# Kernel optimization log

Hardware: AMD Instinct MI355X
Metric: run time of the kernel (lower is better)

Reference implementation:

```python
import jax, jax.numpy as jnp
import numpy as np

N, D, K = 65536, 64, 128   # points, feature dim, n_clusters
BETA = 0.0                 # distance weighting exponent offset
EPS = 1e-8


def pairwise_distance(a, b):
    # euclidean distance matrix [n, k]
    d2 = jnp.sum(a * a, 1)[:, None] + jnp.sum(b * b, 1)[None, :] - 2.0 * (a @ b.T)
    return jnp.sqrt(jnp.maximum(d2, 0.0))


def approx_cluster_filling(dist, beta):
    # differentiable soft cluster filling: inverse-distance weights with exponent (1+beta),
    # normalized per point, averaged over points -> [K]
    w = (dist + EPS) ** (-(1.0 + beta))
    w = w / jnp.sum(w, axis=1, keepdims=True)
    return jnp.mean(w, axis=0)


def wasserstein_distance(a, b):
    # sort-based per-feature 1D Wasserstein-1 distance, averaged over features
    return jnp.mean(jnp.abs(jnp.sort(a, axis=0) - jnp.sort(b, axis=0)))


def setup_inputs():
    key = jax.random.key(0)
    k1, k2, k3 = jax.random.split(key, 3)
    x = jax.random.normal(k1, (N, D), jnp.float32)
    target = jax.random.normal(k2, (N, D), jnp.float32)
    cluster_centers = jax.random.normal(k3, (K, D), jnp.float32)
    # precomputed target-side cluster statistics (LossKMeans.__init__, detached)
    dist_t = pairwise_distance(target, cluster_centers)
    prediction_target = jnp.argmin(dist_t, axis=1).astype(jnp.int32)
    filling_target = approx_cluster_filling(dist_t, BETA)
    return {"x": x, "target": target, "cluster_centers": cluster_centers,
            "prediction_target": prediction_target, "filling_target": filling_target}


def reference(x, target, cluster_centers, prediction_target, filling_target):
    # cluster-filling MSE (differentiable soft assignment)
    dist_x = pairwise_distance(x, cluster_centers)
    loss_fil = jnp.mean((approx_cluster_filling(dist_x, BETA) - filling_target) ** 2)
    # hard (detached) cluster assignment of x; concrete in eager mode
    pred_x = np.asarray(jnp.argmin(dist_x, axis=1))
    pred_t = np.asarray(prediction_target)
    loss_med = jnp.zeros((), jnp.float32)
    for c in np.unique(pred_x):  # data-dependent loop over occupied clusters (<= K)
        ix = np.nonzero(pred_x == c)[0]
        it = np.nonzero(pred_t == c)[0]
        m = min(ix.size, it.size)
        if m == 0:
            continue  # no matching target members -> skip (empty slices)
        loss_med = loss_med + wasserstein_distance(x[ix[:m]], target[it[:m]])
    return loss_fil + loss_med
```

## Files before the change

### kernel.cpp

```cpp
#include <hip/hip_runtime.h>
#include <math.h>

#define N_PTS 65536
#define DIM   64
#define K_CL  128
#define EPSV  1e-8f
#define CAP   8192


__global__ __launch_bounds__(256) void k_init(
    float* __restrict__ fill_acc, float* __restrict__ sumw,
    unsigned long long* __restrict__ pred_enc) {
  const int i = blockIdx.x * 256 + threadIdx.x;
  if (i < K_CL) fill_acc[i] = 0.0f;
  sumw[i] = 0.0f;
  pred_enc[i] = 0xFFFFFFFFFFFFFFFFull;
}

__global__ __launch_bounds__(256) void k_dist1(
    const float* __restrict__ x, const float* __restrict__ centers,
    float* __restrict__ sumw, unsigned long long* __restrict__ pred_enc,
    float* __restrict__ w)
{
  __shared__ float csq[32];
  const int kb    = blockIdx.x & 3;
  const int pb    = blockIdx.x >> 2;
  const int jbase = kb << 5;
  const int tid   = threadIdx.x;
  const int p     = pb * 256 + tid;

  if (tid < 32) {
    const float* cp = centers + (jbase + tid) * DIM;
    float s = 0.0f;
    #pragma unroll 8
    for (int d = 0; d < DIM; ++d) { float v = cp[d]; s += v * v; }
    csq[tid] = s;
  }

  float xr[DIM];
  const float4* xp = reinterpret_cast<const float4*>(x + (size_t)p * DIM);
  #pragma unroll
  for (int q = 0; q < DIM / 4; ++q) {
    float4 v = xp[q];
    xr[4 * q + 0] = v.x; xr[4 * q + 1] = v.y;
    xr[4 * q + 2] = v.z; xr[4 * q + 3] = v.w;
  }
  float xsq = 0.0f;
  #pragma unroll
  for (int d = 0; d < DIM; ++d) xsq += xr[d] * xr[d];
  __syncthreads();

  float sw = 0.0f, best = INFINITY;
  int   bj = jbase;
  #pragma unroll 2
  for (int jj = 0; jj < 32; ++jj) {
    const int j = jbase + jj;
    const float* cp = centers + j * DIM;
    float d0 = 0.f, d1 = 0.f, d2a = 0.f, d3 = 0.f;
    #pragma unroll
    for (int d = 0; d < DIM; d += 4) {
      d0  += xr[d + 0] * cp[d + 0];
      d1  += xr[d + 1] * cp[d + 1];
      d2a += xr[d + 2] * cp[d + 2];
      d3  += xr[d + 3] * cp[d + 3];
    }
    float dot  = (d0 + d1) + (d2a + d3);
    float dsq  = xsq + csq[jj] - 2.0f * dot;
    float dist = sqrtf(fmaxf(dsq, 0.0f));
    float ww   = 1.0f / (dist + EPSV);
    w[(size_t)j * N_PTS + p] = ww;
    sw += ww;
    if (dist < best) { best = dist; bj = j; }
  }
  atomicAdd(&sumw[p], sw);
  const unsigned long long enc =
      ((unsigned long long)__float_as_uint(best) << 32) | (unsigned int)bj;
  atomicMin(&pred_enc[p], enc);
}

__global__ __launch_bounds__(256) void k_pred(
    const unsigned long long* __restrict__ pred_enc,
    const float* __restrict__ sumw,
    int* __restrict__ pred_x, float* __restrict__ inv_sumw) {
  const int p = blockIdx.x * 256 + threadIdx.x;
  pred_x[p]   = (int)(pred_enc[p] & 0xFFFFFFFFull);
  inv_sumw[p] = 1.0f / sumw[p];
}

__global__ __launch_bounds__(256) void k_fill(
    const float* __restrict__ w, const float* __restrict__ inv_sumw,
    float* __restrict__ fill_acc)
{
  __shared__ float red[4];
  const int j    = blockIdx.x >> 3;
  const int seg  = blockIdx.x & 7;
  const int tid  = threadIdx.x;
  const float4* wj = reinterpret_cast<const float4*>(
      w + (size_t)j * N_PTS + seg * 8192);
  const float4* iv = reinterpret_cast<const float4*>(inv_sumw + seg * 8192);
  float s = 0.0f;
  #pragma unroll
  for (int q = 0; q < 8; ++q) {
    const int e = q * 256 + tid;
    float4 a = wj[e];
    float4 b = iv[e];
    s += a.x * b.x + a.y * b.y + a.z * b.z + a.w * b.w;
  }
  #pragma unroll
  for (int off = 32; off > 0; off >>= 1) s += __shfl_down(s, off);
  if ((tid & 63) == 0) red[tid >> 6] = s;
  __syncthreads();
  if (tid == 0)
    atomicAdd(&fill_acc[j], red[0] + red[1] + red[2] + red[3]);
}

__global__ __launch_bounds__(1024) void k_scatter(
    const int* __restrict__ pred_x, const int* __restrict__ pred_t,
    int* __restrict__ idx_x, int* __restrict__ idx_t,
    int* __restrict__ count_x, int* __restrict__ count_t)
{
  const int c    = blockIdx.x >> 1;
  const int side = blockIdx.x & 1;
  const int* __restrict__ pred = side ? pred_t : pred_x;
  int* __restrict__ out = side ? idx_t : idx_x;
  int* __restrict__ cnt = side ? count_t : count_x;

  __shared__ int wsum[16];
  const int tid = threadIdx.x, lane = tid & 63, w = tid >> 6;
  const int beg = w * 4096;

  int cw = 0;
  for (int s = 0; s < 4096; s += 64) {
    const bool m = (pred[beg + s + lane] == c);
    cw += __popcll(__ballot(m));
  }
  if (lane == 0) wsum[w] = cw;
  __syncthreads();
  int base = 0, tot = 0;
  #pragma unroll
  for (int k = 0; k < 16; ++k) { int v = wsum[k]; tot += v; if (k < w) base += v; }

  int run = base;
  for (int s = 0; s < 4096; s += 64) {
    const int i = beg + s + lane;
    const bool m = (pred[i] == c);
    unsigned long long bal = __ballot(m);
    int lp = __popcll(bal & ((1ull << lane) - 1ull));
    if (m) { int pos = run + lp; if (pos < CAP) out[c * CAP + pos] = i; }
    run += __popcll(bal);
  }
  if (tid == 0) cnt[c] = tot;
}

__global__ __launch_bounds__(128) void k_offsets(
    const int* __restrict__ count_x, const int* __restrict__ count_t,
    int* __restrict__ offc)
{
  __shared__ int sm[128];
  const int tid = threadIdx.x;
  const int m  = min(min(count_x[tid], CAP), min(count_t[tid], CAP));
  const int sz = ((m + 3) & ~3) * DIM;
  sm[tid] = sz;
  __syncthreads();
  for (int s = 1; s < 128; s <<= 1) {
    int v = (tid >= s) ? sm[tid - s] : 0;
    __syncthreads();
    sm[tid] += v;
    __syncthreads();
  }
  offc[tid] = sm[tid] - sz;
}

__global__ __launch_bounds__(256) void k_gather_t(
    const float* __restrict__ x, const float* __restrict__ t,
    const int* __restrict__ idx_x, const int* __restrict__ idx_t,
    const int* __restrict__ count_x, const int* __restrict__ count_t,
    const int* __restrict__ offc,
    float* __restrict__ gxT, float* __restrict__ gtT)
{
  const int wid  = blockIdx.x * 4 + (threadIdx.x >> 6);
  const int lane = threadIdx.x & 63;
  const int side = wid >> 14;
  const int c    = (wid >> 7) & 127;
  const int q    = wid & 127;
  const int m = min(min(count_x[c], CAP), min(count_t[c], CAP));
  if (q * 64 >= m) return;
  const int r  = q * 64 + lane;
  const int mp = (m + 3) & ~3;
  const float* __restrict__ src = side ? t : x;
  const int*   __restrict__ idx = side ? idx_t : idx_x;
  float* __restrict__ dst = (side ? gtT : gxT) + offc[c];
  if (r < m) {
    const float4* rp =
        reinterpret_cast<const float4*>(src + (size_t)idx[c * CAP + r] * DIM);
    float v[DIM];
    #pragma unroll
    for (int qq = 0; qq < DIM / 4; ++qq) {
      float4 f = rp[qq];
      v[4*qq+0]=f.x; v[4*qq+1]=f.y; v[4*qq+2]=f.z; v[4*qq+3]=f.w;
    }
    #pragma unroll
    for (int d = 0; d < DIM; ++d) dst[(size_t)d * mp + r] = v[d];
  }
}

__device__ __forceinline__ void ce(float& a, float& b, bool up) {
  float lo = fminf(a, b), hi = fmaxf(a, b);
  a = up ? lo : hi;
  b = up ? hi : lo;
}

__device__ __forceinline__ void merge8(float* v, bool up) {
  ce(v[0],v[4],up); ce(v[1],v[5],up); ce(v[2],v[6],up); ce(v[3],v[7],up);
  ce(v[0],v[2],up); ce(v[1],v[3],up); ce(v[4],v[6],up); ce(v[5],v[7],up);
  ce(v[0],v[1],up); ce(v[2],v[3],up); ce(v[4],v[5],up); ce(v[6],v[7],up);
}

__device__ __forceinline__ void sort8(float* v, bool up8) {
  ce(v[0],v[1],true );  ce(v[2],v[3],false); ce(v[4],v[5],true );  ce(v[6],v[7],false);
  ce(v[0],v[2],true );  ce(v[1],v[3],true );  ce(v[4],v[6],false); ce(v[5],v[7],false);
  ce(v[0],v[1],true );  ce(v[2],v[3],true );  ce(v[4],v[5],false); ce(v[6],v[7],false);
  merge8(v, up8);
}

__device__ __forceinline__ void merge16(float* v, bool up) {
  #pragma unroll
  for (int e = 0; e < 8; ++e) ce(v[e], v[e + 8], up);
  merge8(v, up);
  merge8(v + 8, up);
}

__device__ __forceinline__ void sort16(float* v, bool up16) {
  sort8(v, true);
  sort8(v + 8, false);
  merge16(v, up16);
}

__device__ __forceinline__ void stage_one8(float v[8], int ib, int k, bool up) {
  for (int j = (k >> 1) > 256 ? 256 : (k >> 1); j >= 8; j >>= 1) {
    const int  jl = j >> 3;
    const bool tm = (up == ((ib & j) == 0));
    #pragma unroll
    for (int e = 0; e < 8; ++e) {
      float p = __shfl_xor(v[e], jl, 64);
      v[e] = tm ? fminf(v[e], p) : fmaxf(v[e], p);
    }
  }
  merge8(v, up);
}

__device__ __forceinline__ void stage_one16(float v[16], int ib, int k, bool up) {
  #pragma unroll
  for (int j = (k >> 1) > 512 ? 512 : (k >> 1); j >= 16; j >>= 1) {
    const int  jl = j >> 4;
    const bool tm = (up == ((ib & j) == 0));
    #pragma unroll
    for (int e = 0; e < 16; ++e) {
      float p = __shfl_xor(v[e], jl, 64);
      v[e] = tm ? fminf(v[e], p) : fmaxf(v[e], p);
    }
  }
  merge16(v, up);
}

__device__ __forceinline__ void load8c(const float* __restrict__ col,
                                       int ib, int m, float v[8]) {
  if (ib + 7 < m) {
    #pragma unroll
    for (int q = 0; q < 2; ++q) {
      float4 f = *(const float4*)&col[ib + 4 * q];
      v[4*q+0]=f.x; v[4*q+1]=f.y; v[4*q+2]=f.z; v[4*q+3]=f.w;
    }
  } else {
    #pragma unroll
    for (int e = 0; e < 8; ++e) v[e] = (ib + e < m) ? col[ib + e] : INFINITY;
  }
}

__device__ __forceinline__ void load16c(const float* __restrict__ col,
                                        int ib, int m, float v[16]) {
  if (ib + 15 < m) {
    #pragma unroll
    for (int q = 0; q < 4; ++q) {
      float4 f = *(const float4*)&col[ib + 4 * q];
      v[4*q+0]=f.x; v[4*q+1]=f.y; v[4*q+2]=f.z; v[4*q+3]=f.w;
    }
  } else {
    #pragma unroll
    for (int e = 0; e < 16; ++e) v[e] = (ib + e < m) ? col[ib + e] : INFINITY;
  }
}

template<int P>
__device__ __forceinline__ void sort_col(float v[16], int ib, bool act,
                                         const float* __restrict__ col,
                                         int m, float* __restrict__ sa) {
  if (act) {
    load16c(col, ib, m, v);
    sort16(v, ((ib & 16) == 0));
    #pragma unroll
    for (int k = 32; k <= 1024; k <<= 1)
      stage_one16(v, ib, k, ((ib & k) == 0));
  }
  #pragma unroll
  for (int k = 2048; k <= P; k <<= 1) {
    const bool up = ((ib & k) == 0);
    #pragma unroll
    for (int j = k >> 1; j >= 1024; j >>= 1) {
      __syncthreads();
      if (act) {
        #pragma unroll
        for (int q = 0; q < 4; ++q)
          *(float4*)&sa[ib + 4*q] =
              make_float4(v[4*q], v[4*q+1], v[4*q+2], v[4*q+3]);
      }
      __syncthreads();
      if (act) {
        const int pi = ib ^ j;
        const bool tm = (up == ((ib & j) == 0));
        #pragma unroll
        for (int q = 0; q < 4; ++q) {
          float4 A = *(const float4*)&sa[pi + 4*q];
          v[4*q+0] = tm ? fminf(v[4*q+0],A.x) : fmaxf(v[4*q+0],A.x);
          v[4*q+1] = tm ? fminf(v[4*q+1],A.y) : fmaxf(v[4*q+1],A.y);
          v[4*q+2] = tm ? fminf(v[4*q+2],A.z) : fmaxf(v[4*q+2],A.z);
          v[4*q+3] = tm ? fminf(v[4*q+3],A.w) : fmaxf(v[4*q+3],A.w);
        }
      }
    }
    if (act) stage_one16(v, ib, k, up);
  }
}

template<int P>
__device__ __forceinline__ void sort_col_io(float* __restrict__ col,
                                            int m, int mp, int tid,
                                            float* __restrict__ sa) {
  const int ib = tid << 4;
  const bool act = (ib < P);
  float v[16];
  sort_col<P>(v, ib, act, col, m, sa);
  if (act) {
    #pragma unroll
    for (int q = 0; q < 4; ++q)
      if (ib + 4 * q < mp)
        *(float4*)&col[ib + 4*q] =
            make_float4(v[4*q], v[4*q+1], v[4*q+2], v[4*q+3]);
  }
}

__global__ __launch_bounds__(512) void k_sort(
    float* __restrict__ gxT, float* __restrict__ gtT,
    const int* __restrict__ offc,
    const int* __restrict__ count_x, const int* __restrict__ count_t)
{
  __shared__ float sa[8192];
  const int tid = threadIdx.x;

  if (blockIdx.x < 16384) {
    const int side = blockIdx.x >> 13;
    const int cd   = blockIdx.x & 8191;
    const int c = cd >> 6, d = cd & 63;
    const int m = min(min(count_x[c], CAP), min(count_t[c], CAP));
    if (m <= 1024) return;
    const int mp = (m + 3) & ~3;
    float* col = (side ? gtT : gxT) + offc[c] + (size_t)d * mp;
    if (m <= 2048)      sort_col_io<2048>(col, m, mp, tid, sa);
    else if (m <= 4096) sort_col_io<4096>(col, m, mp, tid, sa);
    else                sort_col_io<8192>(col, m, mp, tid, sa);
  } else {
    const int base = (blockIdx.x - 16384) * 8 + (tid >> 6);
    const int lane = tid & 63;
    const int side = base >> 13;
    const int cd   = base & 8191;
    const int c = cd >> 6, d = cd & 63;
    const int m = min(min(count_x[c], CAP), min(count_t[c], CAP));
    if (m > 1024 || m == 0) return;
    const int mp = (m + 3) & ~3;
    float* col = (side ? gtT : gxT) + offc[c] + (size_t)d * mp;

    if (m <= 512) {
      int P = 8;
      while (P < m) P <<= 1;
      const int ib = lane << 3;
      float v[8];
      load8c(col, ib, m, v);
      sort8(v, ((ib & 8) == 0));
      for (int k = 16; k <= P; k <<= 1)
        stage_one8(v, ib, k, ((ib & k) == 0));
      #pragma unroll
      for (int q = 0; q < 2; ++q)
        if (ib + 4 * q < mp)
          *(float4*)&col[ib + 4*q] =
              make_float4(v[4*q], v[4*q+1], v[4*q+2], v[4*q+3]);
    } else {
      const int ib = lane << 4;
      float v[16];
      load16c(col, ib, m, v);
      sort16(v, ((ib & 16) == 0));
      #pragma unroll
      for (int k = 32; k <= 1024; k <<= 1)
        stage_one16(v, ib, k, ((ib & k) == 0));
      #pragma unroll
      for (int q = 0; q < 4; ++q)
        if (ib + 4 * q < mp)
          *(float4*)&col[ib + 4*q] =
              make_float4(v[4*q], v[4*q+1], v[4*q+2], v[4*q+3]);
    }
  }
}

__global__ __launch_bounds__(256) void k_diff(
    const float* __restrict__ gxT, const float* __restrict__ gtT,
    const int* __restrict__ offc,
    const int* __restrict__ count_x, const int* __restrict__ count_t,
    float* __restrict__ parts)
{
  __shared__ float red[4];
  const int task = blockIdx.x;
  const int c = task >> 6, d = task & 63;
  const int m = min(min(count_x[c], CAP), min(count_t[c], CAP));
  const int tid = threadIdx.x;
  if (m == 0) { if (tid == 0) parts[task] = 0.0f; return; }
  const int mp = (m + 3) & ~3;
  const float* colx = gxT + offc[c] + (size_t)d * mp;
  const float* colt = gtT + offc[c] + (size_t)d * mp;
  float s = 0.0f;
  for (int r = tid * 4; r < mp; r += 1024) {
    float4 a = *(const float4*)&colx[r];
    float4 b = *(const float4*)&colt[r];
    if (r + 3 < m) {
      s += fabsf(a.x-b.x) + fabsf(a.y-b.y) + fabsf(a.z-b.z) + fabsf(a.w-b.w);
    } else {
      if (r + 0 < m) s += fabsf(a.x - b.x);
      if (r + 1 < m) s += fabsf(a.y - b.y);
      if (r + 2 < m) s += fabsf(a.z - b.z);
      if (r + 3 < m) s += fabsf(a.w - b.w);
    }
  }
  #pragma unroll
  for (int off = 32; off > 0; off >>= 1) s += __shfl_down(s, off);
  if ((tid & 63) == 0) red[tid >> 6] = s;
  __syncthreads();
  if (tid == 0)
    parts[task] = (red[0] + red[1] + red[2] + red[3]) / (float)(m * DIM);
}

__global__ __launch_bounds__(1024) void k_final(
    const float* __restrict__ fill_acc, const float* __restrict__ ft,
    const float* __restrict__ parts, float* __restrict__ out)
{
  __shared__ float red[16];
  const int tid = threadIdx.x;
  float s = 0.0f;
  #pragma unroll
  for (int i = 0; i < 8; ++i) s += parts[tid + i * 1024];
  if (tid < K_CL) {
    float v = fill_acc[tid] * (1.0f / (float)N_PTS) - ft[tid];
    s += v * v * (1.0f / (float)K_CL);
  }
  #pragma unroll
  for (int off = 32; off > 0; off >>= 1) s += __shfl_down(s, off);
  if ((tid & 63) == 0) red[tid >> 6] = s;
  __syncthreads();
  if (tid == 0) {
    float tot = 0.0f;
    #pragma unroll
    for (int w = 0; w < 16; ++w) tot += red[w];
    out[0] = tot;
  }
}

extern "C" void kernel_launch(void* const* d_in, const int* in_sizes, int n_in,
                              void* d_out, int out_size, void* d_ws, size_t ws_size,
                              hipStream_t stream)
{
  (void)in_sizes; (void)n_in; (void)out_size; (void)ws_size;
  const float* x      = (const float*)d_in[0];
  const float* target = (const float*)d_in[1];
  const float* cc     = (const float*)d_in[2];
  const int*   pred_t = (const int*)d_in[3];
  const float* ft     = (const float*)d_in[4];
  float* out = (float*)d_out;

  char* ws = (char*)d_ws;
  float* fill_acc = (float*)(ws + 0);
  int*   pred_x   = (int*)(ws + 1024);
  int*   idx_x    = (int*)(ws + 263168);
  int*   idx_t    = (int*)(ws + 4457472);
  int*   count_x  = (int*)(ws + 8651776);
  int*   count_t  = (int*)(ws + 8651776 + 512);
  float* parts    = (float*)(ws + 8652800);
  float* sumw     = (float*)(ws + 8685568);
  float* inv_sumw = (float*)(ws + 8947712);
  unsigned long long* pred_enc = (unsigned long long*)(ws + 9209856);
  int*   offc     = (int*)(ws + 9734144);
  float* gxT      = (float*)(ws + 9735168);
  float* gtT      = (float*)(ws + 26643456);
  float* wmat     = (float*)(ws + 9735168);

  k_init<<<N_PTS / 256, 256, 0, stream>>>(fill_acc, sumw, pred_enc);
  k_dist1<<<N_PTS / 256 * 4, 256, 0, stream>>>(x, cc, sumw, pred_enc, wmat);
  k_pred<<<N_PTS / 256, 256, 0, stream>>>(pred_enc, sumw, pred_x, inv_sumw);
  k_fill<<<K_CL * 8, 256, 0, stream>>>(wmat, inv_sumw, fill_acc);
  k_scatter<<<K_CL * 2, 1024, 0, stream>>>(pred_x, pred_t, idx_x, idx_t,
                                           count_x, count_t);
  k_offsets<<<1, 128, 0, stream>>>(count_x, count_t, offc);
  k_gather_t<<<8192, 256, 0, stream>>>(x, target, idx_x, idx_t,
                                       count_x, count_t, offc, gxT, gtT);
  k_sort<<<16384 + 2048, 512, 0, stream>>>(gxT, gtT, offc, count_x, count_t);
  k_diff<<<K_CL * DIM, 256, 0, stream>>>(gxT, gtT, offc,
                                         count_x, count_t, parts);
  k_final<<<1, 1024, 0, stream>>>(fill_acc, ft, parts, out);
}
```

Baseline: 322.8 us.

## Pack multiple columns per block in large-column bitonic sort and swizzle LDS

For columns of 1025–4096 elements, the sort kernel now packs 4 (or 2) columns into one 512-thread block, so every thread is active instead of most idling. Blocks whose column index is not a multiple of the pack factor exit early. Shared-memory accesses in the cross-thread merge stages use an XOR swizzle to reduce bank conflicts. The cost is more early-exit blocks, and each block's shared buffer is split across sub-columns.

```diff
diff --git a/kernel.cpp b/kernel.cpp
--- a/kernel.cpp
+++ b/kernel.cpp
@@ -291,62 +291,50 @@
   }
 }
 
-template<int P>
-__device__ __forceinline__ void sort_col(float v[16], int ib, bool act,
-                                         const float* __restrict__ col,
-                                         int m, float* __restrict__ sa) {
-  if (act) {
-    load16c(col, ib, m, v);
-    sort16(v, ((ib & 16) == 0));
-    #pragma unroll
-    for (int k = 32; k <= 1024; k <<= 1)
-      stage_one16(v, ib, k, ((ib & k) == 0));
-  }
+__device__ __forceinline__ int swz4(int fi) {
+  return fi ^ (((fi >> 5) & 7) << 2);
+}
+
+template<int P, int T>
+__device__ __forceinline__ void sort_col_packed(float* __restrict__ col,
+                                                int m, int mp, int lt,
+                                                float* __restrict__ sa) {
+  const int ib = lt << 4;
+  float v[16];
+  load16c(col, ib, m, v);
+  sort16(v, ((ib & 16) == 0));
+  #pragma unroll
+  for (int k = 32; k <= 1024; k <<= 1)
+    stage_one16(v, ib, k, ((ib & k) == 0));
   #pragma unroll
   for (int k = 2048; k <= P; k <<= 1) {
     const bool up = ((ib & k) == 0);
     #pragma unroll
     for (int j = k >> 1; j >= 1024; j >>= 1) {
       __syncthreads();
-      if (act) {
-        #pragma unroll
-        for (int q = 0; q < 4; ++q)
-          *(float4*)&sa[ib + 4*q] =
-              make_float4(v[4*q], v[4*q+1], v[4*q+2], v[4*q+3]);
+      #pragma unroll
+      for (int q = 0; q < 4; ++q)
+        *(float4*)&sa[swz4(ib + 4 * q)] =
+            make_float4(v[4*q], v[4*q+1], v[4*q+2], v[4*q+3]);
+      __syncthreads();
+      const int pi = ib ^ j;
+      const bool tm = (up == ((ib & j) == 0));
+      #pragma unroll
+      for (int q = 0; q < 4; ++q) {
+        float4 A = *(const float4*)&sa[swz4(pi + 4 * q)];
+        v[4*q+0] = tm ? fminf(v[4*q+0],A.x) : fmaxf(v[4*q+0],A.x);
+        v[4*q+1] = tm ? fminf(v[4*q+1],A.y) : fmaxf(v[4*q+1],A.y);
+        v[4*q+2] = tm ? fminf(v[4*q+2],A.z) : fmaxf(v[4*q+2],A.z);
+        v[4*q+3] = tm ? fminf(v[4*q+3],A.w) : fmaxf(v[4*q+3],A.w);
       }
-      __syncthreads();
-      if (act) {
-        const int pi = ib ^ j;
-        const bool tm = (up == ((ib & j) == 0));
-        #pragma unroll
-        for (int q = 0; q < 4; ++q) {
-          float4 A = *(const float4*)&sa[pi + 4*q];
-          v[4*q+0] = tm ? fminf(v[4*q+0],A.x) : fmaxf(v[4*q+0],A.x);
-          v[4*q+1] = tm ? fminf(v[4*q+1],A.y) : fmaxf(v[4*q+1],A.y);
-          v[4*q+2] = tm ? fminf(v[4*q+2],A.z) : fmaxf(v[4*q+2],A.z);
-          v[4*q+3] = tm ? fminf(v[4*q+3],A.w) : fmaxf(v[4*q+3],A.w);
-        }
-      }
-    }
-    if (act) stage_one16(v, ib, k, up);
-  }
-}
-
-template<int P>
-__device__ __forceinline__ void sort_col_io(float* __restrict__ col,
-                                            int m, int mp, int tid,
-                                            float* __restrict__ sa) {
-  const int ib = tid << 4;
-  const bool act = (ib < P);
-  float v[16];
-  sort_col<P>(v, ib, act, col, m, sa);
-  if (act) {
-    #pragma unroll
-    for (int q = 0; q < 4; ++q)
-      if (ib + 4 * q < mp)
-        *(float4*)&col[ib + 4*q] =
-            make_float4(v[4*q], v[4*q+1], v[4*q+2], v[4*q+3]);
-  }
+    }
+    stage_one16(v, ib, k, up);
+  }
+  #pragma unroll
+  for (int q = 0; q < 4; ++q)
+    if (ib + 4 * q < mp)
+      *(float4*)&col[ib + 4*q] =
+          make_float4(v[4*q], v[4*q+1], v[4*q+2], v[4*q+3]);
 }
 
 __global__ __launch_bounds__(512) void k_sort(
@@ -364,10 +352,20 @@
     const int m = min(min(count_x[c], CAP), min(count_t[c], CAP));
     if (m <= 1024) return;
     const int mp = (m + 3) & ~3;
-    float* col = (side ? gtT : gxT) + offc[c] + (size_t)d * mp;
-    if (m <= 2048)      sort_col_io<2048>(col, m, mp, tid, sa);
-    else if (m <= 4096) sort_col_io<4096>(col, m, mp, tid, sa);
-    else                sort_col_io<8192>(col, m, mp, tid, sa);
+    float* base = (side ? gtT : gxT) + offc[c];
+    if (m <= 2048) {
+      if (d & 3) return;
+      const int sub = tid >> 7, lt = tid & 127;
+      sort_col_packed<2048,128>(base + (size_t)(d + sub) * mp, m, mp, lt,
+                                sa + (sub << 11));
+    } else if (m <= 4096) {
+      if (d & 1) return;
+      const int sub = tid >> 8, lt = tid & 255;
+      sort_col_packed<4096,256>(base + (size_t)(d + sub) * mp, m, mp, lt,
+                                sa + (sub << 12));
+    } else {
+      sort_col_packed<8192,512>(base + (size_t)d * mp, m, mp, tid, sa);
+    }
   } else {
     const int base = (blockIdx.x - 16384) * 8 + (tid >> 6);
     const int lane = tid & 63;
```

New measurement: 360.7 us. 1.12x slower.
